# Kernel tuning notes

Measured on AMD Instinct MI355X. Metric: run time of the kernel, lower is better.

The kernel has to match this reference:

```python
import jax, jax.numpy as jnp
import numpy as np

L, B, T, D = 4, 32, 2048, 100


def setup_inputs() -> dict:
    key = jax.random.key(0)
    k1, k2 = jax.random.split(key)
    h = jax.random.normal(k1, (L, B, T, D), dtype=jnp.float32)
    old_h = jax.random.normal(k2, (L, B, T, D), dtype=jnp.float32)
    layer_weights = jnp.ones((L,), dtype=jnp.float32)
    class_weights = jnp.ones((D,), dtype=jnp.float32)
    return {"h": h, "old_h": old_h, "layer_weights": layer_weights, "class_weights": class_weights}


def reference(h, old_h, layer_weights, class_weights):
    # h, old_h: [L, B, T, D]. Softmax / log_softmax are over the T axis
    # (dim=-1 of h[..., c] which is [B, T]).
    logq = jax.nn.log_softmax(h, axis=2)        # student log-probs  [L,B,T,D]
    logp = jax.nn.log_softmax(old_h, axis=2)    # teacher log-probs  [L,B,T,D]
    p = jnp.exp(logp)                            # teacher probs
    # KL(p || q) per (layer, class), batchmean reduction: sum over (B,T) / B
    kl_lc = jnp.sum(p * (logp - logq), axis=(1, 2)) / jnp.float32(B)  # [L, D]
    lw = jax.nn.softmax(layer_weights)           # [L]
    cw = jax.nn.softmax(class_weights)           # [D]
    loss = jnp.einsum('l,ld,d->', lw, kl_lc, cw)
    return loss
```

## Files before the change

### kernel.cpp

```cpp
#include <hip/hip_runtime.h>

constexpr int kL = 4;
constexpr int kB = 32;
constexpr int kT = 2048;
constexpr int kD = 100;
constexpr int kD4 = kD / 4;
constexpr int kCH = 16;
constexpr int kTSUB = kT / kCH;
constexpr int kROWS = kL * kB * kD;

__global__ __launch_bounds__(256) void kl_partial(
    const float4* __restrict__ h4, const float4* __restrict__ oh4,
    float* __restrict__ wsp, float* __restrict__ wsq, float* __restrict__ ww) {
  const int lb = blockIdx.x >> 4;
  const int chunk = blockIdx.x & 15;
  const int tid = threadIdx.x;
  const int ty = tid >> 6;
  const int lane = tid & 63;
  const int half = lane / kD4;
  const int d4 = lane - half * kD4;
  const bool active = (lane < 2 * kD4);

  float4 sp = {0.f, 0.f, 0.f, 0.f};
  float4 sq = {0.f, 0.f, 0.f, 0.f};
  float4 w  = {0.f, 0.f, 0.f, 0.f};

  if (active) {
    const int row0 = chunk * kTSUB + ty * 2 + half;
    const size_t b4 = ((size_t)lb * kT + row0) * kD4 + d4;
    const float4* __restrict__ hp = h4 + b4;
    const float4* __restrict__ op = oh4 + b4;
#pragma unroll 4
    for (int i = 0; i < kTSUB / 8; ++i) {
      const size_t off = (size_t)i * 8 * kD4;
      const float4 hv = hp[off];
      const float4 ov = op[off];
      const float ep0 = __expf(ov.x), ep1 = __expf(ov.y);
      const float ep2 = __expf(ov.z), ep3 = __expf(ov.w);
      sp.x += ep0; sp.y += ep1; sp.z += ep2; sp.w += ep3;
      sq.x += __expf(hv.x); sq.y += __expf(hv.y);
      sq.z += __expf(hv.z); sq.w += __expf(hv.w);
      w.x += ep0 * (ov.x - hv.x); w.y += ep1 * (ov.y - hv.y);
      w.z += ep2 * (ov.z - hv.z); w.w += ep3 * (ov.w - hv.w);
    }
  }

  __shared__ float red[256][12];
  {
    float* r = red[tid];
    r[0] = sp.x; r[1] = sp.y; r[2]  = sp.z; r[3]  = sp.w;
    r[4] = sq.x; r[5] = sq.y; r[6]  = sq.z; r[7]  = sq.w;
    r[8] = w.x;  r[9] = w.y;  r[10] = w.z;  r[11] = w.w;
  }
  __syncthreads();
  if (tid < kD) {
    const int dd4 = tid >> 2, j = tid & 3;
    float asp = 0.f, asq = 0.f, aw = 0.f;
#pragma unroll
    for (int g = 0; g < 4; ++g) {
#pragma unroll
      for (int hh = 0; hh < 2; ++hh) {
        const float* s = red[g * 64 + hh * kD4 + dd4];
        asp += s[j]; asq += s[4 + j]; aw += s[8 + j];
      }
    }
    const int idx = lb * kD + tid;
    atomicAdd(&wsp[idx], asp);
    atomicAdd(&wsq[idx], asq);
    atomicAdd(&ww[idx],  aw);
  }
}

__global__ __launch_bounds__(256) void kl_reduce(
    const float* __restrict__ wsp, const float* __restrict__ wsq,
    const float* __restrict__ ww, const float* __restrict__ lwin,
    const float* __restrict__ cwin, float* __restrict__ acc) {
  __shared__ float lw[kL];
  __shared__ float cw[kD];
  __shared__ float sred[256];
  const int tid = threadIdx.x;

  if (tid == 0) {
    float m = lwin[0];
    for (int i = 1; i < kL; ++i) m = fmaxf(m, lwin[i]);
    float e[kL], s = 0.f;
    for (int i = 0; i < kL; ++i) { e[i] = __expf(lwin[i] - m); s += e[i]; }
    const float inv = 1.0f / s;
    for (int i = 0; i < kL; ++i) lw[i] = e[i] * inv;
  }
  if (tid == 64) {
    float m = cwin[0];
    for (int i = 1; i < kD; ++i) m = fmaxf(m, cwin[i]);
    float s = 0.f;
    for (int i = 0; i < kD; ++i) { const float e = __expf(cwin[i] - m); cw[i] = e; s += e; }
    const float inv = 1.0f / s;
    for (int i = 0; i < kD; ++i) cw[i] *= inv;
  }
  __syncthreads();

  const int r = blockIdx.x * 256 + tid;
  const int l = r / (kB * kD);
  const int d = r % kD;
  const float spv = wsp[r], sqv = wsq[r], wv = ww[r];
  const float val = wv / spv - __logf(spv) + __logf(sqv);
  sred[tid] = lw[l] * cw[d] * val;
  __syncthreads();
  for (int s = 128; s > 0; s >>= 1) {
    if (tid < s) sred[tid] += sred[tid + s];
    __syncthreads();
  }
  if (tid == 0) atomicAdd(acc, sred[0]);
}

__global__ void kl_write(const float* __restrict__ acc, float* __restrict__ out) {
  out[0] = acc[0] / (float)kB;
}

extern "C" void kernel_launch(void* const* d_in, const int* in_sizes, int n_in,
                              void* d_out, int out_size, void* d_ws, size_t ws_size,
                              hipStream_t stream) {
  const float* h    = (const float*)d_in[0];
  const float* oh   = (const float*)d_in[1];
  const float* lwin = (const float*)d_in[2];
  const float* cwin = (const float*)d_in[3];

  float* wsp = (float*)d_ws;
  float* wsq = wsp + kROWS;
  float* ww  = wsq + kROWS;
  float* acc = ww + kROWS;
  hipMemsetAsync(d_ws, 0, ((size_t)3 * kROWS + 1) * sizeof(float), stream);

  kl_partial<<<kL * kB * kCH, 256, 0, stream>>>(
      (const float4*)h, (const float4*)oh, wsp, wsq, ww);
  kl_reduce<<<kROWS / 256, 256, 0, stream>>>(wsp, wsq, ww, lwin, cwin, acc);
  kl_write<<<1, 1, 0, stream>>>(acc, (float*)d_out);
}
```

Baseline: 243.1 us.

## Double the chunk count, prefetch loads, and replace atomics with per-chunk partials

Splits T into 32 chunks instead of 16, giving twice as many blocks with shorter loops. The streaming loop is fully unrolled with explicit software prefetch of the next float4 pair. Global atomics are replaced by plain stores into per-chunk partial buffers, and the reduce kernel now sums them, so the large memset shrinks to a single float. The trade-off is a larger workspace and extra reads in the reduce kernel.

```diff
diff --git a/kernel.cpp b/kernel.cpp
--- a/kernel.cpp
+++ b/kernel.cpp
@@ -5,15 +5,15 @@
 constexpr int kT = 2048;
 constexpr int kD = 100;
 constexpr int kD4 = kD / 4;
-constexpr int kCH = 16;
+constexpr int kCH = 32;
 constexpr int kTSUB = kT / kCH;
 constexpr int kROWS = kL * kB * kD;
 
 __global__ __launch_bounds__(256) void kl_partial(
     const float4* __restrict__ h4, const float4* __restrict__ oh4,
     float* __restrict__ wsp, float* __restrict__ wsq, float* __restrict__ ww) {
-  const int lb = blockIdx.x >> 4;
-  const int chunk = blockIdx.x & 15;
+  const int lb = blockIdx.x >> 5;
+  const int chunk = blockIdx.x & 31;
   const int tid = threadIdx.x;
   const int ty = tid >> 6;
   const int lane = tid & 63;
@@ -30,18 +30,22 @@
     const size_t b4 = ((size_t)lb * kT + row0) * kD4 + d4;
     const float4* __restrict__ hp = h4 + b4;
     const float4* __restrict__ op = oh4 + b4;
-#pragma unroll 4
-    for (int i = 0; i < kTSUB / 8; ++i) {
-      const size_t off = (size_t)i * 8 * kD4;
-      const float4 hv = hp[off];
-      const float4 ov = op[off];
-      const float ep0 = __expf(ov.x), ep1 = __expf(ov.y);
-      const float ep2 = __expf(ov.z), ep3 = __expf(ov.w);
-      sp.x += ep0; sp.y += ep1; sp.z += ep2; sp.w += ep3;
-      sq.x += __expf(hv.x); sq.y += __expf(hv.y);
-      sq.z += __expf(hv.z); sq.w += __expf(hv.w);
-      w.x += ep0 * (ov.x - hv.x); w.y += ep1 * (ov.y - hv.y);
-      w.z += ep2 * (ov.z - hv.z); w.w += ep3 * (ov.w - hv.w);
+    float4 hc = hp[0];
+    float4 oc = op[0];
+#pragma unroll
+    for (int p = 0; p < kTSUB / 8; ++p) {
+      float4 hn, on;
+      if (p < kTSUB / 8 - 1) {
+        hn = hp[(size_t)(p + 1) * 200];
+        on = op[(size_t)(p + 1) * 200];
+      }
+      const float a = __expf(oc.x), b = __expf(oc.y), c = __expf(oc.z), d = __expf(oc.w);
+      sp.x += a; sp.y += b; sp.z += c; sp.w += d;
+      sq.x += __expf(hc.x); sq.y += __expf(hc.y);
+      sq.z += __expf(hc.z); sq.w += __expf(hc.w);
+      w.x += a * (oc.x - hc.x); w.y += b * (oc.y - hc.y);
+      w.z += c * (oc.z - hc.z); w.w += d * (oc.w - hc.w);
+      if (p < kTSUB / 8 - 1) { hc = hn; oc = on; }
     }
   }
 
@@ -64,10 +68,10 @@
         asp += s[j]; asq += s[4 + j]; aw += s[8 + j];
       }
     }
-    const int idx = lb * kD + tid;
-    atomicAdd(&wsp[idx], asp);
-    atomicAdd(&wsq[idx], asq);
-    atomicAdd(&ww[idx],  aw);
+    const size_t idx = (size_t)chunk * kROWS + lb * kD + tid;
+    wsp[idx] = asp;
+    wsq[idx] = asq;
+    ww[idx]  = aw;
   }
 }
 
@@ -99,9 +103,16 @@
   __syncthreads();
 
   const int r = blockIdx.x * 256 + tid;
+  float spv = 0.f, sqv = 0.f, wv = 0.f;
+#pragma unroll 4
+  for (int c = 0; c < kCH; ++c) {
+    const size_t idx = (size_t)c * kROWS + r;
+    spv += wsp[idx];
+    sqv += wsq[idx];
+    wv  += ww[idx];
+  }
   const int l = r / (kB * kD);
   const int d = r % kD;
-  const float spv = wsp[r], sqv = wsq[r], wv = ww[r];
   const float val = wv / spv - __logf(spv) + __logf(sqv);
   sred[tid] = lw[l] * cw[d] * val;
   __syncthreads();
@@ -125,10 +136,10 @@
   const float* cwin = (const float*)d_in[3];
 
   float* wsp = (float*)d_ws;
-  float* wsq = wsp + kROWS;
-  float* ww  = wsq + kROWS;
-  float* acc = ww + kROWS;
-  hipMemsetAsync(d_ws, 0, ((size_t)3 * kROWS + 1) * sizeof(float), stream);
+  float* wsq = wsp + (size_t)kCH * kROWS;
+  float* ww  = wsq + (size_t)kCH * kROWS;
+  float* acc = ww  + (size_t)kCH * kROWS;
+  hipMemsetAsync(acc, 0, sizeof(float), stream);
 
   kl_partial<<<kL * kB * kCH, 256, 0, stream>>>(
       (const float4*)h, (const float4*)oh, wsp, wsq, ww);
```

Result: no change. 241.5 us (-0.7%).

## Stage input tiles into LDS via direct global-to-LDS loads with larger blocks

Applied to the files above, without the earlier changes.

Replaces per-thread strided float4 global loads with fully coalesced global_load_lds transfers that stage 64-row chunks of h and old_h into shared memory. Threads then read their (row, d4) elements from LDS for the exp/accumulate math. Each block now covers 256 rows instead of 128, halving grid size and atomic traffic. This adds two barriers per chunk and gives no overlap between loading and compute, which could cost latency hiding on a bandwidth-bound kernel.

```diff
diff --git a/kernel.cpp b/kernel.cpp
--- a/kernel.cpp
+++ b/kernel.cpp
@@ -5,52 +5,72 @@
 constexpr int kT = 2048;
 constexpr int kD = 100;
 constexpr int kD4 = kD / 4;
-constexpr int kCH = 16;
-constexpr int kTSUB = kT / kCH;
 constexpr int kROWS = kL * kB * kD;
+constexpr int kRPB = 256;
+constexpr int kRPC = 64;
+constexpr int kNC = kRPB / kRPC;
+constexpr int kF4C = kRPC * kD4;
+constexpr int kLoads = kF4C / 64;
+
+__device__ __forceinline__ void gload_lds16(const float4* g, float4* l) {
+  __builtin_amdgcn_global_load_lds(
+      (const __attribute__((address_space(1))) void*)g,
+      (__attribute__((address_space(3))) void*)l, 16, 0, 0);
+}
 
 __global__ __launch_bounds__(256) void kl_partial(
     const float4* __restrict__ h4, const float4* __restrict__ oh4,
     float* __restrict__ wsp, float* __restrict__ wsq, float* __restrict__ ww) {
-  const int lb = blockIdx.x >> 4;
-  const int chunk = blockIdx.x & 15;
+  __shared__ float4 smem[2 * kF4C];
+  const int lb = blockIdx.x >> 3;
+  const int blk8 = blockIdx.x & 7;
   const int tid = threadIdx.x;
-  const int ty = tid >> 6;
+  const int wv = tid >> 6;
   const int lane = tid & 63;
   const int half = lane / kD4;
   const int d4 = lane - half * kD4;
-  const bool active = (lane < 2 * kD4);
+  const bool active = lane < 2 * kD4;
+
+  const size_t slab = (size_t)lb * kT * kD4;
+  const int row0 = blk8 * kRPB;
 
   float4 sp = {0.f, 0.f, 0.f, 0.f};
   float4 sq = {0.f, 0.f, 0.f, 0.f};
   float4 w  = {0.f, 0.f, 0.f, 0.f};
 
-  if (active) {
-    const int row0 = chunk * kTSUB + ty * 2 + half;
-    const size_t b4 = ((size_t)lb * kT + row0) * kD4 + d4;
-    const float4* __restrict__ hp = h4 + b4;
-    const float4* __restrict__ op = oh4 + b4;
-#pragma unroll 4
-    for (int i = 0; i < kTSUB / 8; ++i) {
-      const size_t off = (size_t)i * 8 * kD4;
-      const float4 hv = hp[off];
-      const float4 ov = op[off];
-      const float ep0 = __expf(ov.x), ep1 = __expf(ov.y);
-      const float ep2 = __expf(ov.z), ep3 = __expf(ov.w);
-      sp.x += ep0; sp.y += ep1; sp.z += ep2; sp.w += ep3;
-      sq.x += __expf(hv.x); sq.y += __expf(hv.y);
-      sq.z += __expf(hv.z); sq.w += __expf(hv.w);
-      w.x += ep0 * (ov.x - hv.x); w.y += ep1 * (ov.y - hv.y);
-      w.z += ep2 * (ov.z - hv.z); w.w += ep3 * (ov.w - hv.w);
+  for (int c = 0; c < kNC; ++c) {
+    const size_t cbase = slab + (size_t)(row0 + c * kRPC) * kD4;
+    const float4* gh = h4 + cbase + lane;
+    const float4* go = oh4 + cbase + lane;
+    for (int j = wv; j < kLoads; j += 4) {
+      gload_lds16(gh + j * 64, smem + j * 64 + lane);
+      gload_lds16(go + j * 64, smem + kF4C + j * 64 + lane);
     }
+    __syncthreads();
+    if (active) {
+#pragma unroll
+      for (int p = 0; p < 8; ++p) {
+        const int r = 2 * wv + half + 8 * p;
+        const float4 hv = smem[r * kD4 + d4];
+        const float4 ov = smem[kF4C + r * kD4 + d4];
+        const float a = __expf(ov.x), b = __expf(ov.y),
+                    cc = __expf(ov.z), dd = __expf(ov.w);
+        sp.x += a; sp.y += b; sp.z += cc; sp.w += dd;
+        sq.x += __expf(hv.x); sq.y += __expf(hv.y);
+        sq.z += __expf(hv.z); sq.w += __expf(hv.w);
+        w.x += a * (ov.x - hv.x); w.y += b * (ov.y - hv.y);
+        w.z += cc * (ov.z - hv.z); w.w += dd * (ov.w - hv.w);
+      }
+    }
+    __syncthreads();
   }
 
-  __shared__ float red[256][12];
+  float* red = (float*)smem;
   {
-    float* r = red[tid];
-    r[0] = sp.x; r[1] = sp.y; r[2]  = sp.z; r[3]  = sp.w;
-    r[4] = sq.x; r[5] = sq.y; r[6]  = sq.z; r[7]  = sq.w;
-    r[8] = w.x;  r[9] = w.y;  r[10] = w.z;  r[11] = w.w;
+    float* rr = red + tid * 12;
+    rr[0] = sp.x; rr[1] = sp.y; rr[2]  = sp.z; rr[3]  = sp.w;
+    rr[4] = sq.x; rr[5] = sq.y; rr[6]  = sq.z; rr[7]  = sq.w;
+    rr[8] = w.x;  rr[9] = w.y;  rr[10] = w.z;  rr[11] = w.w;
   }
   __syncthreads();
   if (tid < kD) {
@@ -60,7 +80,7 @@
     for (int g = 0; g < 4; ++g) {
 #pragma unroll
       for (int hh = 0; hh < 2; ++hh) {
-        const float* s = red[g * 64 + hh * kD4 + dd4];
+        const float* s = red + (g * 64 + hh * kD4 + dd4) * 12;
         asp += s[j]; asq += s[4 + j]; aw += s[8 + j];
       }
     }
@@ -130,7 +150,7 @@
   float* acc = ww + kROWS;
   hipMemsetAsync(d_ws, 0, ((size_t)3 * kROWS + 1) * sizeof(float), stream);
 
-  kl_partial<<<kL * kB * kCH, 256, 0, stream>>>(
+  kl_partial<<<kL * kB * (kT / kRPB), 256, 0, stream>>>(
       (const float4*)h, (const float4*)oh, wsp, wsq, ww);
   kl_reduce<<<kROWS / 256, 256, 0, stream>>>(wsp, wsq, ww, lwin, cwin, acc);
   kl_write<<<1, 1, 0, stream>>>(acc, (float*)d_out);
```

New measurement: 245.2 us. No clear change (+0.9%).
